# Kernel optimization log

Measured on AMD Instinct MI355X. Metric: run time of the kernel, lower is better.

The kernel has to match this reference:

```python
import jax, jax.numpy as jnp
import numpy as np

NUM_HEADS = 16


def _make_rope(n, half_dim, dtype=jnp.float32):
    # standard rotary frequencies: theta = 10000^{-2i/d}
    inv_freq = 1.0 / (10000.0 ** (np.arange(0, half_dim, dtype=np.float32) / half_dim))
    t = np.arange(n, dtype=np.float32)
    ang = np.outer(t, inv_freq)  # [n, half_dim]
    return jnp.asarray(np.cos(ang), dtype), jnp.asarray(np.sin(ang), dtype)


def setup_inputs() -> dict:
    key = jax.random.key(0)
    ks = jax.random.split(key, 10)
    B, N, C = 2, 2048, 1024
    H = NUM_HEADS
    hd = C // H
    q = jax.random.normal(ks[0], (B, N, C), jnp.float32)
    k = jax.random.normal(ks[1], (B, N, C), jnp.float32)
    v = jax.random.normal(ks[2], (B, N, C), jnp.float32)
    cos, sin = _make_rope(N, hd // 2)
    s = 1.0 / np.sqrt(C)
    Wq = jax.random.normal(ks[3], (C, C), jnp.float32) * s
    bq = jax.random.normal(ks[4], (C,), jnp.float32) * 0.02
    Wk = jax.random.normal(ks[5], (C, C), jnp.float32) * s
    bk = jax.random.normal(ks[6], (C,), jnp.float32) * 0.02
    Wv = jax.random.normal(ks[7], (C, C), jnp.float32) * s
    bv = jax.random.normal(ks[8], (C,), jnp.float32) * 0.02
    return {"q": q, "k": k, "v": v,
            "q_cos": cos, "q_sin": sin, "k_cos": cos, "k_sin": sin,
            "Wq": Wq, "bq": bq, "Wk": Wk, "bk": bk, "Wv": Wv, "bv": bv}


def _rope(x, cos, sin):
    # x: [B, H, N, hd]; pairs (x[...,2j], x[...,2j+1]) form complex numbers,
    # rotated by freqs_cis of shape [N, hd//2] (broadcast over B, H).
    xr = x[..., 0::2]
    xi = x[..., 1::2]
    c = cos[None, None]  # [1,1,N,hd//2]
    s = sin[None, None]
    out_r = xr * c - xi * s
    out_i = xr * s + xi * c
    return jnp.stack([out_r, out_i], axis=-1).reshape(x.shape)


def reference(q, k, v, q_cos, q_sin, k_cos, k_sin, Wq, bq, Wk, bk, Wv, bv):
    B, Nq, C = q.shape
    Nk = k.shape[1]
    H = NUM_HEADS
    hd = C // H
    scale = hd ** -0.5
    # QKV projections (torch nn.Linear: x @ W.T + b), split into heads
    qh = (q @ Wq.T + bq).reshape(B, Nq, H, hd).transpose(0, 2, 1, 3)  # [B,H,Nq,hd]
    kh = (k @ Wk.T + bk).reshape(B, Nk, H, hd).transpose(0, 2, 1, 3)
    vh = (v @ Wv.T + bv).reshape(B, Nk, H, hd).transpose(0, 2, 1, 3)
    # inline RoPE on q and k
    qh = _rope(qh, q_cos, q_sin)
    kh = _rope(kh, k_cos, k_sin)
    # scaled dot-product attention (mask=None, dropout=0, non-causal)
    scores = jnp.einsum('bhqd,bhkd->bhqk', qh, kh) * scale
    attn = jax.nn.softmax(scores, axis=-1)
    out = jnp.einsum('bhqk,bhkd->bhqd', attn, vh)
    # merge heads; NOTE: self.proj is never applied in the original forward
    return out.transpose(0, 2, 1, 3).reshape(B, Nq, C)
```

## Files before the change

### kernel.cpp

```cpp
#include <hip/hip_runtime.h>
#include <hip/hip_bf16.h>

typedef float f32x4 __attribute__((ext_vector_type(4)));
typedef float f32x16 __attribute__((ext_vector_type(16)));
typedef short bf16x8 __attribute__((ext_vector_type(8)));

#define NSEQ 2048
#define CDIM 1024
#define NHEAD 16
#define HDIM 64
#define MROWS 4096
#define QSCALE 0.18033688011f
#define DEFER_THR 11.5416f

__device__ __forceinline__ unsigned short f2bf(float f) {
    unsigned int u = __builtin_bit_cast(unsigned int, f);
    u += 0x7FFFu + ((u >> 16) & 1u);
    return (unsigned short)(u >> 16);
}

__device__ __forceinline__ unsigned pkbf(float lo, float hi_) {
    unsigned r;
    asm("v_cvt_pk_bf16_f32 %0, %1, %2" : "=v"(r) : "v"(lo), "v"(hi_));
    return r;
}

__device__ __forceinline__ void gload16(const void* g, void* l) {
    __builtin_amdgcn_global_load_lds(
        (const __attribute__((address_space(1))) unsigned int*)g,
        (__attribute__((address_space(3))) unsigned int*)l, 16, 0, 0);
}

__global__ __launch_bounds__(256) void cvt6_kernel(
    const float* __restrict__ q, const float* __restrict__ k, const float* __restrict__ v,
    const float* __restrict__ wq, const float* __restrict__ wk, const float* __restrict__ wv,
    unsigned short* __restrict__ dq, unsigned short* __restrict__ dk, unsigned short* __restrict__ dv,
    unsigned short* __restrict__ dwq, unsigned short* __restrict__ dwk, unsigned short* __restrict__ dwv)
{
    int b = blockIdx.x;
    const float* s; unsigned short* d; int base;
    if (b < 4096)       { s = q;  d = dq;  base = b; }
    else if (b < 8192)  { s = k;  d = dk;  base = b - 4096; }
    else if (b < 12288) { s = v;  d = dv;  base = b - 8192; }
    else if (b < 13312) { s = wq; d = dwq; base = b - 12288; }
    else if (b < 14336) { s = wk; d = dwk; base = b - 13312; }
    else                { s = wv; d = dwv; base = b - 14336; }
    int i = (base * 256 + threadIdx.x) * 4;
    float4 t4 = *reinterpret_cast<const float4*>(s + i);
    ushort4 o;
    o.x = f2bf(t4.x); o.y = f2bf(t4.y); o.z = f2bf(t4.z); o.w = f2bf(t4.w);
    *reinterpret_cast<ushort4*>(d + i) = o;
}

__global__ __launch_bounds__(256) void gemm_rope_kernel(
    const unsigned short* __restrict__ Xq, const unsigned short* __restrict__ Xk,
    const unsigned short* __restrict__ Xv,
    const unsigned short* __restrict__ Wqb, const unsigned short* __restrict__ Wkb,
    const unsigned short* __restrict__ Wvb,
    const float* __restrict__ bq, const float* __restrict__ bk, const float* __restrict__ bv,
    const float* __restrict__ qcos, const float* __restrict__ qsin,
    const float* __restrict__ kcos, const float* __restrict__ ksin,
    unsigned short* __restrict__ Qh, unsigned short* __restrict__ Kh,
    unsigned short* __restrict__ VT)
{
    __shared__ unsigned short Al[128][64];
    __shared__ unsigned short Bl[128][64];

    const int tid  = threadIdx.x;
    const int wave = tid >> 6;
    const int lane = tid & 63;
    const int lr   = lane & 15;
    const int lg   = lane >> 4;
    const int wm   = wave >> 1;
    const int wn   = wave & 1;
    const int m0   = blockIdx.y * 128;
    const int j0   = blockIdx.x * 128;
    const int z    = blockIdx.z;

    const unsigned short* X = (z == 0) ? Xq : (z == 1) ? Xk : Xv;
    const unsigned short* W = (z == 0) ? Wqb : (z == 1) ? Wkb : Wvb;
    const float* bias = (z == 0) ? bq : (z == 1) ? bk : bv;
    const float* cosb = (z == 0) ? qcos : kcos;
    const float* sinb = (z == 0) ? qsin : ksin;

    const int srow = lane >> 3;
    const int scol = (lane & 7) * 16;

    f32x4 acc[4][4];
    const f32x4 zero4 = {0.f, 0.f, 0.f, 0.f};
    #pragma unroll
    for (int a = 0; a < 4; a++)
        #pragma unroll
        for (int b = 0; b < 4; b++) acc[a][b] = zero4;

    for (int k0 = 0; k0 < CDIM; k0 += 64) {
        __syncthreads();
        #pragma unroll
        for (int i = 0; i < 4; i++) {
            const int ch  = wave * 4 + i;
            const int row = ch * 8 + srow;
            gload16((const char*)X + ((size_t)(m0 + row) * CDIM + k0) * 2 + scol,
                    (char*)&Al[0][0] + ch * 1024);
            gload16((const char*)W + ((size_t)(j0 + row) * CDIM + k0) * 2 + scol,
                    (char*)&Bl[0][0] + ch * 1024);
        }
        __syncthreads();
        #pragma unroll
        for (int ks = 0; ks < 2; ks++) {
            bf16x8 af[4], bfm[4];
            #pragma unroll
            for (int mi = 0; mi < 4; mi++)
                af[mi] = *reinterpret_cast<const bf16x8*>(
                    (char*)&Al[0][0] + (wm * 64 + 16 * mi + lr) * 128 + ks * 64 + lg * 16);
            #pragma unroll
            for (int ni = 0; ni < 4; ni++)
                bfm[ni] = *reinterpret_cast<const bf16x8*>(
                    (char*)&Bl[0][0] + (wn * 64 + 16 * ni + lr) * 128 + ks * 64 + lg * 16);
            #pragma unroll
            for (int mi = 0; mi < 4; mi++)
                #pragma unroll
                for (int ni = 0; ni < 4; ni++)
                    acc[mi][ni] = __builtin_amdgcn_mfma_f32_16x16x32_bf16(
                        af[mi], bfm[ni], acc[mi][ni], 0, 0, 0);
        }
    }

    #pragma unroll
    for (int mi = 0; mi < 4; mi++) {
        const int mbase = m0 + wm * 64 + 16 * mi + 4 * lg;
        #pragma unroll
        for (int ni = 0; ni < 4; ni++) {
            const int j  = j0 + wn * 64 + 16 * ni + lr;
            const float bj = bias[j];
            if (z == 2) {
                const int b = mbase >> 11, n = mbase & 2047;
                const int h = j >> 6, d = j & 63;
                ushort4 pk;
                pk.x = f2bf(acc[mi][ni][0] + bj);
                pk.y = f2bf(acc[mi][ni][1] + bj);
                pk.z = f2bf(acc[mi][ni][2] + bj);
                pk.w = f2bf(acc[mi][ni][3] + bj);
                *reinterpret_cast<ushort4*>(VT + ((size_t)((b * NHEAD + h) * HDIM + d) << 11) + n) = pk;
            } else {
                unsigned short* Out = (z == 0) ? Qh : Kh;
                const float scl = (z == 0) ? QSCALE : 1.0f;
                const int hi = (j & 63) >> 1;
                const float sg = (j & 1) ? 1.f : -1.f;
                float vv[4], pp[4];
                #pragma unroll
                for (int r = 0; r < 4; r++) vv[r] = acc[mi][ni][r] + bj;
                #pragma unroll
                for (int r = 0; r < 4; r++) pp[r] = __shfl_xor(vv[r], 1);
                #pragma unroll
                for (int r = 0; r < 4; r++) {
                    const int m = mbase + r;
                    const int b = m >> 11, n = m & 2047;
                    const float c = cosb[n * 32 + hi];
                    const float s = sinb[n * 32 + hi];
                    const float ov = fmaf(vv[r], c, pp[r] * (sg * s)) * scl;
                    Out[((size_t)((b * NHEAD + (j >> 6)) * NSEQ + n) << 6) + (j & 63)] = f2bf(ov);
                }
            }
        }
    }
}

__global__ __launch_bounds__(256, 2) void attn_kernel(
    const unsigned short* __restrict__ Qh, const unsigned short* __restrict__ Kh,
    const unsigned short* __restrict__ VT, float* __restrict__ out)
{
    __shared__ unsigned char Ksm[3][8192];
    __shared__ unsigned char Vsm[3][8192];

    const int tid  = threadIdx.x;
    const int wave = tid >> 6;
    const int lane = tid & 63;
    const int c    = lane & 31;
    const int hi   = lane >> 5;
    const int bh   = blockIdx.y;
    const int q0w  = blockIdx.x * 128 + wave * 32;
    const int sw   = (c & 7) << 4;

    const unsigned short* Qb = Qh + (size_t)bh * NSEQ * HDIM;
    const char* Kb = (const char*)(Kh + (size_t)bh * NSEQ * HDIM);
    const char* Vb = (const char*)(VT + (size_t)bh * HDIM * NSEQ);

    bf16x8 qf[4];
    #pragma unroll
    for (int s = 0; s < 4; s++)
        qf[s] = *reinterpret_cast<const bf16x8*>(
            Qb + (size_t)(q0w + c) * HDIM + s * 16 + hi * 8);

    const f32x16 z16 = {0,0,0,0,0,0,0,0,0,0,0,0,0,0,0,0};
    f32x16 o0 = z16, o1 = z16;
    float mrun = -1e30f, lrun = 0.f;

    const int sr7 = lane >> 3;
    const int scb = ((lane & 7) * 16) ^ (sr7 << 4);
    const int ch0 = wave * 2;

    auto stage = [&](int buf, int n0) {
        #pragma unroll
        for (int i = 0; i < 2; ++i) {
            const int row = (ch0 + i) * 8 + sr7;
            gload16(Kb + (size_t)(n0 + row) * 128 + scb, &Ksm[buf][(ch0 + i) * 1024]);
            gload16(Vb + (size_t)row * (NSEQ * 2) + (size_t)n0 * 2 + scb,
                    &Vsm[buf][(ch0 + i) * 1024]);
        }
    };

    stage(0, 0);
    stage(1, 64);

    for (int t = 0; t < 32; ++t) {
        const int cur = t % 3;
        __builtin_amdgcn_s_barrier();
        if (t < 30) {
            stage((t + 2) % 3, (t + 2) * 64);
            asm volatile("s_waitcnt vmcnt(8)" ::: "memory");
        } else if (t == 30) {
            asm volatile("s_waitcnt vmcnt(4)" ::: "memory");
        } else {
            asm volatile("s_waitcnt vmcnt(0)" ::: "memory");
        }
        __builtin_amdgcn_s_barrier();

        f32x16 s0 = z16, s1 = z16;
        __builtin_amdgcn_s_setprio(1);
        #pragma unroll
        for (int s = 0; s < 4; s++) {
            const int cb = (32 * s + 16 * hi) ^ sw;
            bf16x8 kf0 = *reinterpret_cast<const bf16x8*>(&Ksm[cur][c * 128 + cb]);
            bf16x8 kf1 = *reinterpret_cast<const bf16x8*>(&Ksm[cur][(32 + c) * 128 + cb]);
            s0 = __builtin_amdgcn_mfma_f32_32x32x16_bf16(kf0, qf[s], s0, 0, 0, 0);
            s1 = __builtin_amdgcn_mfma_f32_32x32x16_bf16(kf1, qf[s], s1, 0, 0, 0);
        }
        __builtin_amdgcn_s_setprio(0);

        float tmx[8];
        #pragma unroll
        for (int i = 0; i < 8; i++)
            tmx[i] = fmaxf(fmaxf(s0[2 * i], s0[2 * i + 1]),
                           fmaxf(s1[2 * i], s1[2 * i + 1]));
        float tm = fmaxf(fmaxf(fmaxf(tmx[0], tmx[1]), fmaxf(tmx[2], tmx[3])),
                         fmaxf(fmaxf(tmx[4], tmx[5]), fmaxf(tmx[6], tmx[7])));
        tm = fmaxf(tm, __shfl_xor(tm, 32));

        if (!__all(tm - mrun <= DEFER_THR)) {
            const float mnew  = fmaxf(mrun, tm);
            const float alpha = exp2f(mrun - mnew);
            mrun = mnew;
            lrun *= alpha;
            #pragma unroll
            for (int r = 0; r < 16; r++) {
                const float ar = __shfl(alpha, (r & 3) + 8 * (r >> 2) + 4 * hi);
                o0[r] *= ar;
                o1[r] *= ar;
            }
        }

        #pragma unroll
        for (int r = 0; r < 16; r++) s0[r] = exp2f(s0[r] - mrun);
        #pragma unroll
        for (int r = 0; r < 16; r++) s1[r] = exp2f(s1[r] - mrun);
        float rsx[8];
        #pragma unroll
        for (int i = 0; i < 8; i++)
            rsx[i] = (s0[2 * i] + s0[2 * i + 1]) + (s1[2 * i] + s1[2 * i + 1]);
        float rs = ((rsx[0] + rsx[1]) + (rsx[2] + rsx[3])) +
                   ((rsx[4] + rsx[5]) + (rsx[6] + rsx[7]));
        rs += __shfl_xor(rs, 32);
        lrun += rs;

        unsigned pw[4][4];
        #pragma unroll
        for (int u = 0; u < 4; u++) {
            const f32x16& sv = (u < 2) ? s0 : s1;
            const int b = (u & 1) * 8;
            unsigned x0 = pkbf(sv[b + 0], sv[b + 1]);
            unsigned y0 = pkbf(sv[b + 4], sv[b + 5]);
            asm("v_permlane32_swap_b32 %0, %1" : "+v"(x0), "+v"(y0));
            unsigned x1 = pkbf(sv[b + 2], sv[b + 3]);
            unsigned y1 = pkbf(sv[b + 6], sv[b + 7]);
            asm("v_permlane32_swap_b32 %0, %1" : "+v"(x1), "+v"(y1));
            pw[u][0] = x0; pw[u][1] = x1; pw[u][2] = y0; pw[u][3] = y1;
        }

        __builtin_amdgcn_s_setprio(1);
        #pragma unroll
        for (int u = 0; u < 4; u++) {
            uint4 w;
            w.x = pw[u][0]; w.y = pw[u][1]; w.z = pw[u][2]; w.w = pw[u][3];
            bf16x8 pa = __builtin_bit_cast(bf16x8, w);
            const int cb = (32 * u + 16 * hi) ^ sw;
            bf16x8 vf0 = *reinterpret_cast<const bf16x8*>(&Vsm[cur][c * 128 + cb]);
            bf16x8 vf1 = *reinterpret_cast<const bf16x8*>(&Vsm[cur][(32 + c) * 128 + cb]);
            o0 = __builtin_amdgcn_mfma_f32_32x32x16_bf16(pa, vf0, o0, 0, 0, 0);
            o1 = __builtin_amdgcn_mfma_f32_32x32x16_bf16(pa, vf1, o1, 0, 0, 0);
        }
        __builtin_amdgcn_s_setprio(0);
    }

    const int b = bh >> 4, h = bh & 15;
    #pragma unroll
    for (int r = 0; r < 16; r++) {
        const int qrow = (r & 3) + 8 * (r >> 2) + 4 * hi;
        const float li  = __shfl(lrun, qrow);
        const float inv = 1.0f / li;
        const int n = q0w + qrow;
        float* op = out + ((size_t)(b * NSEQ + n) << 10) + h * HDIM + c;
        op[0]  = o0[r] * inv;
        op[32] = o1[r] * inv;
    }
}

extern "C" void kernel_launch(void* const* d_in, const int* in_sizes, int n_in,
                              void* d_out, int out_size, void* d_ws, size_t ws_size,
                              hipStream_t stream) {
    const float* q    = (const float*)d_in[0];
    const float* k    = (const float*)d_in[1];
    const float* v    = (const float*)d_in[2];
    const float* qcos = (const float*)d_in[3];
    const float* qsin = (const float*)d_in[4];
    const float* kcos = (const float*)d_in[5];
    const float* ksin = (const float*)d_in[6];
    const float* Wq   = (const float*)d_in[7];
    const float* bq   = (const float*)d_in[8];
    const float* Wk   = (const float*)d_in[9];
    const float* bk   = (const float*)d_in[10];
    const float* Wv   = (const float*)d_in[11];
    const float* bv   = (const float*)d_in[12];
    float* out = (float*)d_out;

    unsigned short* Xqb = (unsigned short*)d_ws;
    unsigned short* Xkb = Xqb + (size_t)MROWS * CDIM;
    unsigned short* Xvb = Xkb + (size_t)MROWS * CDIM;
    unsigned short* Wqb = Xvb + (size_t)MROWS * CDIM;
    unsigned short* Wkb = Wqb + (size_t)CDIM * CDIM;
    unsigned short* Wvb = Wkb + (size_t)CDIM * CDIM;
    unsigned short* Qhb = Wvb + (size_t)CDIM * CDIM;
    unsigned short* Khb = Qhb + (size_t)MROWS * CDIM;
    unsigned short* VTb = Khb + (size_t)MROWS * CDIM;

    cvt6_kernel<<<15360, 256, 0, stream>>>(q, k, v, Wq, Wk, Wv,
                                           Xqb, Xkb, Xvb, Wqb, Wkb, Wvb);

    dim3 gg(CDIM / 128, MROWS / 128, 3);
    gemm_rope_kernel<<<gg, 256, 0, stream>>>(Xqb, Xkb, Xvb, Wqb, Wkb, Wvb,
                                             bq, bk, bv, qcos, qsin, kcos, ksin,
                                             Qhb, Khb, VTb);

    attn_kernel<<<dim3(NSEQ / 128, 2 * NHEAD), 256, 0, stream>>>(Qhb, Khb, VTb, out);
}
```

Measured before the change: 145.7 us.

## Fuse activation bf16 conversion into GEMM loads and register-stage attention K/V

The separate conversion of q/k/v activations to bf16 is removed. The GEMM now loads fp32 activations directly, packs them to bf16 in registers and writes them into an XOR-swizzled LDS tile, and the fragment reads use the matching swizzle. This drops a full write and reread of the bf16 activation copies, but each GEMM block now reads twice the activation bytes, once per output-column tile. The attention kernel also switches from a 3-buffer async global-to-LDS pipeline to a 2-buffer register-staged prefetch, which lowers LDS use but may expose more load latency.

After: 173.5 us. +19.0%, slower.

```diff
diff --git a/kernel.cpp b/kernel.cpp
--- a/kernel.cpp
+++ b/kernel.cpp
@@ -31,20 +31,16 @@
         (__attribute__((address_space(3))) unsigned int*)l, 16, 0, 0);
 }
 
-__global__ __launch_bounds__(256) void cvt6_kernel(
-    const float* __restrict__ q, const float* __restrict__ k, const float* __restrict__ v,
+__global__ __launch_bounds__(256) void cvt3_kernel(
     const float* __restrict__ wq, const float* __restrict__ wk, const float* __restrict__ wv,
-    unsigned short* __restrict__ dq, unsigned short* __restrict__ dk, unsigned short* __restrict__ dv,
-    unsigned short* __restrict__ dwq, unsigned short* __restrict__ dwk, unsigned short* __restrict__ dwv)
+    unsigned short* __restrict__ dwq, unsigned short* __restrict__ dwk,
+    unsigned short* __restrict__ dwv)
 {
     int b = blockIdx.x;
     const float* s; unsigned short* d; int base;
-    if (b < 4096)       { s = q;  d = dq;  base = b; }
-    else if (b < 8192)  { s = k;  d = dk;  base = b - 4096; }
-    else if (b < 12288) { s = v;  d = dv;  base = b - 8192; }
-    else if (b < 13312) { s = wq; d = dwq; base = b - 12288; }
-    else if (b < 14336) { s = wk; d = dwk; base = b - 13312; }
-    else                { s = wv; d = dwv; base = b - 14336; }
+    if (b < 1024)      { s = wq; d = dwq; base = b; }
+    else if (b < 2048) { s = wk; d = dwk; base = b - 1024; }
+    else               { s = wv; d = dwv; base = b - 2048; }
     int i = (base * 256 + threadIdx.x) * 4;
     float4 t4 = *reinterpret_cast<const float4*>(s + i);
     ushort4 o;
@@ -53,8 +49,8 @@
 }
 
 __global__ __launch_bounds__(256) void gemm_rope_kernel(
-    const unsigned short* __restrict__ Xq, const unsigned short* __restrict__ Xk,
-    const unsigned short* __restrict__ Xv,
+    const float* __restrict__ Xq, const float* __restrict__ Xk,
+    const float* __restrict__ Xv,
     const unsigned short* __restrict__ Wqb, const unsigned short* __restrict__ Wkb,
     const unsigned short* __restrict__ Wvb,
     const float* __restrict__ bq, const float* __restrict__ bk, const float* __restrict__ bv,
@@ -63,8 +59,8 @@
     unsigned short* __restrict__ Qh, unsigned short* __restrict__ Kh,
     unsigned short* __restrict__ VT)
 {
-    __shared__ unsigned short Al[128][64];
-    __shared__ unsigned short Bl[128][64];
+    __shared__ unsigned char Asm[16384];
+    __shared__ unsigned char Bsm[16384];
 
     const int tid  = threadIdx.x;
     const int wave = tid >> 6;
@@ -77,14 +73,17 @@
     const int j0   = blockIdx.x * 128;
     const int z    = blockIdx.z;
 
-    const unsigned short* X = (z == 0) ? Xq : (z == 1) ? Xk : Xv;
+    const float* X = (z == 0) ? Xq : (z == 1) ? Xk : Xv;
     const unsigned short* W = (z == 0) ? Wqb : (z == 1) ? Wkb : Wvb;
     const float* bias = (z == 0) ? bq : (z == 1) ? bk : bv;
     const float* cosb = (z == 0) ? qcos : kcos;
     const float* sinb = (z == 0) ? qsin : ksin;
 
-    const int srow = lane >> 3;
-    const int scol = (lane & 7) * 16;
+    const int sr7 = lane >> 3;
+    const int scb = ((lane & 7) * 16) ^ (sr7 << 4);
+    const int asc   = tid & 7;
+    const int aswz  = (asc * 16) ^ (((tid >> 3) & 7) << 4);
+    const int fsw = (lr & 7) << 4;
 
     f32x4 acc[4][4];
     const f32x4 zero4 = {0.f, 0.f, 0.f, 0.f};
@@ -98,11 +97,20 @@
         #pragma unroll
         for (int i = 0; i < 4; i++) {
             const int ch  = wave * 4 + i;
-            const int row = ch * 8 + srow;
-            gload16((const char*)X + ((size_t)(m0 + row) * CDIM + k0) * 2 + scol,
-                    (char*)&Al[0][0] + ch * 1024);
-            gload16((const char*)W + ((size_t)(j0 + row) * CDIM + k0) * 2 + scol,
-                    (char*)&Bl[0][0] + ch * 1024);
+            const int row = ch * 8 + sr7;
+            gload16((const char*)W + ((size_t)(j0 + row) * CDIM + k0) * 2 + scb,
+                    Bsm + ch * 1024);
+        }
+        #pragma unroll
+        for (int i = 0; i < 4; i++) {
+            const int row = (i * 256 + tid) >> 3;
+            const float4* px = reinterpret_cast<const float4*>(
+                X + (size_t)(m0 + row) * CDIM + k0 + asc * 8);
+            float4 a = px[0], b = px[1];
+            uint4 w;
+            w.x = pkbf(a.x, a.y); w.y = pkbf(a.z, a.w);
+            w.z = pkbf(b.x, b.y); w.w = pkbf(b.z, b.w);
+            *reinterpret_cast<uint4*>(&Asm[row * 128 + aswz]) = w;
         }
         __syncthreads();
         #pragma unroll
@@ -111,11 +119,11 @@
             #pragma unroll
             for (int mi = 0; mi < 4; mi++)
                 af[mi] = *reinterpret_cast<const bf16x8*>(
-                    (char*)&Al[0][0] + (wm * 64 + 16 * mi + lr) * 128 + ks * 64 + lg * 16);
+                    &Asm[(wm * 64 + 16 * mi + lr) * 128 + ((ks * 64 + lg * 16) ^ fsw)]);
             #pragma unroll
             for (int ni = 0; ni < 4; ni++)
                 bfm[ni] = *reinterpret_cast<const bf16x8*>(
-                    (char*)&Bl[0][0] + (wn * 64 + 16 * ni + lr) * 128 + ks * 64 + lg * 16);
+                    &Bsm[(wn * 64 + 16 * ni + lr) * 128 + ((ks * 64 + lg * 16) ^ fsw)]);
             #pragma unroll
             for (int mi = 0; mi < 4; mi++)
                 #pragma unroll
@@ -169,8 +177,8 @@
     const unsigned short* __restrict__ Qh, const unsigned short* __restrict__ Kh,
     const unsigned short* __restrict__ VT, float* __restrict__ out)
 {
-    __shared__ unsigned char Ksm[3][8192];
-    __shared__ unsigned char Vsm[3][8192];
+    __shared__ unsigned char Ksm[2][8192];
+    __shared__ unsigned char Vsm[2][8192];
 
     const int tid  = threadIdx.x;
     const int wave = tid >> 6;
@@ -195,35 +203,35 @@
     f32x16 o0 = z16, o1 = z16;
     float mrun = -1e30f, lrun = 0.f;
 
-    const int sr7 = lane >> 3;
-    const int scb = ((lane & 7) * 16) ^ (sr7 << 4);
-    const int ch0 = wave * 2;
-
-    auto stage = [&](int buf, int n0) {
+    const int sc16 = (tid & 7) * 16;
+    const int swsl = sc16 ^ (((tid >> 3) & 7) << 4);
+
+    uint4 kr[2], vr[2];
+    auto issue = [&](int n0) {
         #pragma unroll
         for (int i = 0; i < 2; ++i) {
-            const int row = (ch0 + i) * 8 + sr7;
-            gload16(Kb + (size_t)(n0 + row) * 128 + scb, &Ksm[buf][(ch0 + i) * 1024]);
-            gload16(Vb + (size_t)row * (NSEQ * 2) + (size_t)n0 * 2 + scb,
-                    &Vsm[buf][(ch0 + i) * 1024]);
+            const int row = (i * 256 + tid) >> 3;
+            kr[i] = *reinterpret_cast<const uint4*>(Kb + (size_t)(n0 + row) * 128 + sc16);
+            vr[i] = *reinterpret_cast<const uint4*>(Vb + (size_t)row * (NSEQ * 2) +
+                                                    (size_t)n0 * 2 + sc16);
         }
     };
-
-    stage(0, 0);
-    stage(1, 64);
+    auto write = [&](int buf) {
+        #pragma unroll
+        for (int i = 0; i < 2; ++i) {
+            const int row = (i * 256 + tid) >> 3;
+            *reinterpret_cast<uint4*>(&Ksm[buf][row * 128 + swsl]) = kr[i];
+            *reinterpret_cast<uint4*>(&Vsm[buf][row * 128 + swsl]) = vr[i];
+        }
+    };
+
+    issue(0);
+    write(0);
+    issue(64);
+    asm volatile("s_waitcnt lgkmcnt(0)\n\ts_barrier" ::: "memory");
 
     for (int t = 0; t < 32; ++t) {
-        const int cur = t % 3;
-        __builtin_amdgcn_s_barrier();
-        if (t < 30) {
-            stage((t + 2) % 3, (t + 2) * 64);
-            asm volatile("s_waitcnt vmcnt(8)" ::: "memory");
-        } else if (t == 30) {
-            asm volatile("s_waitcnt vmcnt(4)" ::: "memory");
-        } else {
-            asm volatile("s_waitcnt vmcnt(0)" ::: "memory");
-        }
-        __builtin_amdgcn_s_barrier();
+        const int cur = t & 1;
 
         f32x16 s0 = z16, s1 = z16;
         __builtin_amdgcn_s_setprio(1);
@@ -299,6 +307,12 @@
             o1 = __builtin_amdgcn_mfma_f32_32x32x16_bf16(pa, vf1, o1, 0, 0, 0);
         }
         __builtin_amdgcn_s_setprio(0);
+
+        if (t < 31) {
+            write(cur ^ 1);
+            if (t < 30) issue((t + 2) * 64);
+            asm volatile("s_waitcnt lgkmcnt(0)\n\ts_barrier" ::: "memory");
+        }
     }
 
     const int b = bh >> 4, h = bh & 15;
@@ -332,21 +346,17 @@
     const float* bv   = (const float*)d_in[12];
     float* out = (float*)d_out;
 
-    unsigned short* Xqb = (unsigned short*)d_ws;
-    unsigned short* Xkb = Xqb + (size_t)MROWS * CDIM;
-    unsigned short* Xvb = Xkb + (size_t)MROWS * CDIM;
-    unsigned short* Wqb = Xvb + (size_t)MROWS * CDIM;
+    unsigned short* Wqb = (unsigned short*)d_ws;
     unsigned short* Wkb = Wqb + (size_t)CDIM * CDIM;
     unsigned short* Wvb = Wkb + (size_t)CDIM * CDIM;
     unsigned short* Qhb = Wvb + (size_t)CDIM * CDIM;
     unsigned short* Khb = Qhb + (size_t)MROWS * CDIM;
     unsigned short* VTb = Khb + (size_t)MROWS * CDIM;
 
-    cvt6_kernel<<<15360, 256, 0, stream>>>(q, k, v, Wq, Wk, Wv,
-                                           Xqb, Xkb, Xvb, Wqb, Wkb, Wvb);
+    cvt3_kernel<<<3072, 256, 0, stream>>>(Wq, Wk, Wv, Wqb, Wkb, Wvb);
 
     dim3 gg(CDIM / 128, MROWS / 128, 3);
-    gemm_rope_kernel<<<gg, 256, 0, stream>>>(Xqb, Xkb, Xvb, Wqb, Wkb, Wvb,
+    gemm_rope_kernel<<<gg, 256, 0, stream>>>(q, k, v, Wqb, Wkb, Wvb,
                                              bq, bk, bv, qcos, qsin, kcos, ksin,
                                              Qhb, Khb, VTb);
 
```
